# Kernel optimization log

Measured on AMD Instinct MI355X. Metric: run time of the kernel, lower is better.

The kernel has to match this reference:

```python
import jax, jax.numpy as jnp
import numpy as np

B, N, C = 4096, 49, 128
NUM_HEADS = 4
SCALE = C ** (-0.5)  # NOTE: source uses dim**-0.5, not head_dim**-0.5


def setup_inputs() -> dict:
    key = jax.random.key(0)
    k1, k2, k3 = jax.random.split(key, 3)
    x = jax.random.normal(k1, (B, N, C), dtype=jnp.float32)
    Wqkv = jax.random.normal(k2, (C, 3 * C), dtype=jnp.float32) * 0.02
    bqkv = jnp.zeros((3 * C,), dtype=jnp.float32)
    Wproj = jax.random.normal(k3, (C, C), dtype=jnp.float32) * 0.02
    bproj = jnp.zeros((C,), dtype=jnp.float32)
    return {"x": x, "Wqkv": Wqkv, "bqkv": bqkv, "Wproj": Wproj, "bproj": bproj}


def reference(x, Wqkv, bqkv, Wproj, bproj):
    b, n, c = x.shape
    h = NUM_HEADS
    d = c // h
    qkv = x @ Wqkv + bqkv                      # [B, N, 3C]
    qkv = qkv.reshape(b, n, 3, h, d).transpose(2, 0, 3, 1, 4)  # [3, B, H, N, d]
    q, k, v = qkv[0], qkv[1], qkv[2]
    attn = jnp.einsum("bhnd,bhmd->bhnm", q, k) * SCALE
    attn = jax.nn.softmax(attn, axis=-1)
    out = jnp.einsum("bhnm,bhmd->bhnd", attn, v)  # [B, H, N, d]
    out = out.transpose(0, 2, 1, 3).reshape(b, n, c)
    return out @ Wproj + bproj
```

## Files before the change

kernel.cpp:

```cpp
#include <hip/hip_runtime.h>


#define N_TOK 49
#define R1B 16384
#define SCF (0.08838834764831845f * 1.4426950408889634f)

typedef __attribute__((ext_vector_type(8))) __bf16 bf16x8;
typedef __attribute__((ext_vector_type(4))) __bf16 bf16x4;
typedef __attribute__((ext_vector_type(4))) float  f32x4;

__global__ void pack_weights(const float* __restrict__ Wqkv,
                             const float* __restrict__ Wproj,
                             __bf16* __restrict__ ws) {
    int idx  = blockIdx.x * 256 + threadIdx.x;
    int j    = idx & 7;
    int lane = (idx >> 3) & 63;
    int l16  = lane & 15, g = lane >> 4;
    if (idx < 49152) {
        int frag = idx >> 9;
        int mt = frag >> 2, ks = frag & 3;
        int m = mt * 16 + l16;
        int k = ks * 32 + g * 8 + j;
        float v = Wqkv[k * 384 + m];
        if (m < 128) v *= SCF;
        ws[idx] = (__bf16)v;
    } else {
        int i2 = idx - 49152;
        int frag = i2 >> 9;
        int nt = frag >> 2, ks = frag & 3;
        int n = nt * 16 + l16;
        int k = ks * 32 + g * 8 + j;
        ws[idx] = (__bf16)Wproj[k * 128 + n];
    }
}

__device__ __forceinline__ int x_off(int tok, int ch) {
    return tok * 256 + ((((ch >> 3) ^ (tok & 15))) << 4) + ((ch & 7) << 1);
}
__device__ __forceinline__ int vt_off(int h, int ch, int tok) {
    return h * 4096 + ch * 128 + ((((tok >> 3) ^ (ch & 7))) << 4) + ((tok & 7) << 1);
}
__device__ __forceinline__ int o_off(int tok, int ch) {
    return (ch >> 5) * 4096 + tok * 64 + (((((ch & 31) >> 3) ^ (tok & 3))) << 4) + ((ch & 7) << 1);
}
__device__ __forceinline__ int k_off(int h, int tok, int ch) {
    return R1B + h * 4096 + tok * 64 + ((((ch >> 3) ^ (tok & 3))) << 4) + ((ch & 7) << 1);
}

__device__ __forceinline__ int pk2(float a, float b) {
    union { __bf16 h[2]; int u; } U;
    U.h[0] = (__bf16)a; U.h[1] = (__bf16)b;
    return U.u;
}

__device__ __forceinline__ bf16x8 reorg8(int m0w0, int m0w1, int m1w0, int m1w1,
                                         int lane) {
    int aA = ((lane & 15) | ((lane & 16) << 1)) << 2;
    int aB = aA + 64;
    int A0 = __builtin_amdgcn_ds_bpermute(aA, m0w0);
    int A1 = __builtin_amdgcn_ds_bpermute(aA, m0w1);
    int B0 = __builtin_amdgcn_ds_bpermute(aB, m0w0);
    int B1 = __builtin_amdgcn_ds_bpermute(aB, m0w1);
    int C0 = __builtin_amdgcn_ds_bpermute(aA, m1w0);
    int C1 = __builtin_amdgcn_ds_bpermute(aA, m1w1);
    int D0 = __builtin_amdgcn_ds_bpermute(aB, m1w0);
    int D1 = __builtin_amdgcn_ds_bpermute(aB, m1w1);
    bool hi = lane >= 32;
    union { int u[4]; bf16x8 v; } U;
    U.u[0] = hi ? C0 : A0;
    U.u[1] = hi ? C1 : A1;
    U.u[2] = hi ? D0 : B0;
    U.u[3] = hi ? D1 : B1;
    return U.v;
}

__global__ __launch_bounds__(256, 4)
void fused_win_attn(const float* __restrict__ x,
                    const float* __restrict__ bqkv,
                    const float* __restrict__ bproj,
                    const __bf16* __restrict__ wpack,
                    float* __restrict__ out) {
    __shared__ __align__(16) char smem[32768];

    const int tid  = threadIdx.x;
    const int w    = tid >> 6;
    const int lane = tid & 63;
    const int l16  = lane & 15;
    const int g    = lane >> 4;
    const int b    = blockIdx.x;
    const float* xb = x + (size_t)b * (N_TOK * 128);

    #pragma unroll
    for (int it = 0; it < 4; ++it) {
        int unit = tid + it * 256;
        int tok = unit >> 4, ch = (unit & 15) * 8;
        f32x4 lo = {0.f, 0.f, 0.f, 0.f}, hi = {0.f, 0.f, 0.f, 0.f};
        if (tok < N_TOK) {
            const float* p = xb + tok * 128 + ch;
            lo = *(const f32x4*)p;
            hi = *(const f32x4*)(p + 4);
        }
        bf16x8 f;
        f[0]=(__bf16)lo[0]; f[1]=(__bf16)lo[1]; f[2]=(__bf16)lo[2]; f[3]=(__bf16)lo[3];
        f[4]=(__bf16)hi[0]; f[5]=(__bf16)hi[1]; f[6]=(__bf16)hi[2]; f[7]=(__bf16)hi[3];
        *(bf16x8*)(smem + x_off(tok, ch)) = f;
    }
    __syncthreads();

    f32x4 bq0 = *(const f32x4*)(bqkv + 32 * w + 0 + 4 * g);   bq0 *= SCF;
    f32x4 bq1 = *(const f32x4*)(bqkv + 32 * w + 16 + 4 * g);  bq1 *= SCF;
    f32x4 bk0 = *(const f32x4*)(bqkv + 128 + 32 * w + 0 + 4 * g);
    f32x4 bk1 = *(const f32x4*)(bqkv + 128 + 32 * w + 16 + 4 * g);
    f32x4 accA[4][4];
    #pragma unroll
    for (int nt = 0; nt < 4; ++nt) {
        accA[0][nt] = bq0; accA[1][nt] = bq1;
        accA[2][nt] = bk0; accA[3][nt] = bk1;
    }
    #pragma unroll
    for (int ks = 0; ks < 4; ++ks) {
        bf16x8 xfr[4];
        #pragma unroll
        for (int nt = 0; nt < 4; ++nt)
            xfr[nt] = *(const bf16x8*)(smem + x_off(16 * nt + l16, 32 * ks + 8 * g));
        #pragma unroll
        for (int m = 0; m < 4; ++m) {
            int mtg = (m < 2) ? (2 * w + m) : (8 + 2 * w + m - 2);
            bf16x8 af = *(const bf16x8*)(wpack + ((mtg * 4 + ks) * 64 + lane) * 8);
            #pragma unroll
            for (int nt = 0; nt < 4; ++nt)
                accA[m][nt] = __builtin_amdgcn_mfma_f32_16x16x32_bf16(af, xfr[nt], accA[m][nt], 0, 0, 0);
        }
    }
    #pragma unroll
    for (int m = 2; m < 4; ++m) {
        const int lch = 16 * (m - 2) + 4 * g;
        #pragma unroll
        for (int nt = 0; nt < 4; ++nt) {
            bf16x4 pk = {(__bf16)accA[m][nt][0], (__bf16)accA[m][nt][1],
                         (__bf16)accA[m][nt][2], (__bf16)accA[m][nt][3]};
            *(bf16x4*)(smem + k_off(w, 16 * nt + l16, lch)) = pk;
        }
    }
    bf16x8 qf[4];
    #pragma unroll
    for (int t = 0; t < 4; ++t) {
        int m0w0 = pk2(accA[0][t][0], accA[0][t][1]);
        int m0w1 = pk2(accA[0][t][2], accA[0][t][3]);
        int m1w0 = pk2(accA[1][t][0], accA[1][t][1]);
        int m1w1 = pk2(accA[1][t][2], accA[1][t][3]);
        qf[t] = reorg8(m0w0, m0w1, m1w0, m1w1, lane);
    }

    f32x4 bv0 = *(const f32x4*)(bqkv + 256 + 32 * w + 0 + 4 * g);
    f32x4 bv1 = *(const f32x4*)(bqkv + 256 + 32 * w + 16 + 4 * g);
    f32x4 accB[2][4];
    #pragma unroll
    for (int nt = 0; nt < 4; ++nt) { accB[0][nt] = bv0; accB[1][nt] = bv1; }
    #pragma unroll
    for (int ks = 0; ks < 4; ++ks) {
        bf16x8 xfr[4];
        #pragma unroll
        for (int nt = 0; nt < 4; ++nt)
            xfr[nt] = *(const bf16x8*)(smem + x_off(16 * nt + l16, 32 * ks + 8 * g));
        #pragma unroll
        for (int m = 0; m < 2; ++m) {
            bf16x8 af = *(const bf16x8*)(wpack + (((16 + 2 * w + m) * 4 + ks) * 64 + lane) * 8);
            #pragma unroll
            for (int nt = 0; nt < 4; ++nt)
                accB[m][nt] = __builtin_amdgcn_mfma_f32_16x16x32_bf16(af, xfr[nt], accB[m][nt], 0, 0, 0);
        }
    }
    __syncthreads();

    #pragma unroll
    for (int m = 0; m < 2; ++m) {
        const int vch = 16 * m + 4 * g;
        #pragma unroll
        for (int nt = 0; nt < 4; ++nt) {
            const int T = 16 * nt + l16;
            *(__bf16*)(smem + vt_off(w, vch + 0, T)) = (__bf16)accB[m][nt][0];
            *(__bf16*)(smem + vt_off(w, vch + 1, T)) = (__bf16)accB[m][nt][1];
            *(__bf16*)(smem + vt_off(w, vch + 2, T)) = (__bf16)accB[m][nt][2];
            *(__bf16*)(smem + vt_off(w, vch + 3, T)) = (__bf16)accB[m][nt][3];
        }
    }

    f32x4 s[4][4];
    #pragma unroll
    for (int mt = 0; mt < 4; ++mt) {
        bf16x8 kf = *(const bf16x8*)(smem + k_off(w, 16 * mt + l16, 8 * g));
        #pragma unroll
        for (int nt = 0; nt < 4; ++nt)
            s[mt][nt] = __builtin_amdgcn_mfma_f32_16x16x32_bf16(
                kf, qf[nt], (f32x4){0.f, 0.f, 0.f, 0.f}, 0, 0, 0);
    }

    float r[4];
    #pragma unroll
    for (int nt = 0; nt < 4; ++nt) {
        float sum = 0.f;
        #pragma unroll
        for (int mt = 0; mt < 4; ++mt)
            #pragma unroll
            for (int i = 0; i < 4; ++i) {
                int key = 16 * mt + 4 * g + i;
                float p = (key < N_TOK) ? __builtin_amdgcn_exp2f(s[mt][nt][i]) : 0.f;
                s[mt][nt][i] = p;
                sum += p;
            }
        sum += __shfl_xor(sum, 16);
        sum += __shfl_xor(sum, 32);
        r[nt] = __builtin_amdgcn_rcpf(sum);
    }

    bf16x8 pf[4][2];
    #pragma unroll
    for (int nt = 0; nt < 4; ++nt)
        #pragma unroll
        for (int ks = 0; ks < 2; ++ks) {
            int m0w0 = pk2(s[2 * ks][nt][0], s[2 * ks][nt][1]);
            int m0w1 = pk2(s[2 * ks][nt][2], s[2 * ks][nt][3]);
            int m1w0 = pk2(s[2 * ks + 1][nt][0], s[2 * ks + 1][nt][1]);
            int m1w1 = pk2(s[2 * ks + 1][nt][2], s[2 * ks + 1][nt][3]);
            pf[nt][ks] = reorg8(m0w0, m0w1, m1w0, m1w1, lane);
        }

    f32x4 o[2][4];
    #pragma unroll
    for (int m = 0; m < 2; ++m)
        #pragma unroll
        for (int nt = 0; nt < 4; ++nt) o[m][nt] = (f32x4){0.f, 0.f, 0.f, 0.f};
    #pragma unroll
    for (int ks = 0; ks < 2; ++ks)
        #pragma unroll
        for (int m = 0; m < 2; ++m) {
            bf16x8 vf = *(const bf16x8*)(smem + vt_off(w, 16 * m + l16, 32 * ks + 8 * g));
            #pragma unroll
            for (int nt = 0; nt < 4; ++nt)
                o[m][nt] = __builtin_amdgcn_mfma_f32_16x16x32_bf16(
                    vf, pf[nt][ks], o[m][nt], 0, 0, 0);
        }

    #pragma unroll
    for (int m = 0; m < 2; ++m)
        #pragma unroll
        for (int nt = 0; nt < 4; ++nt) {
            bf16x4 pk = {(__bf16)(o[m][nt][0] * r[nt]), (__bf16)(o[m][nt][1] * r[nt]),
                         (__bf16)(o[m][nt][2] * r[nt]), (__bf16)(o[m][nt][3] * r[nt])};
            *(bf16x4*)(smem + o_off(16 * nt + l16, 32 * w + 16 * m + 4 * g)) = pk;
        }

    const __bf16* bp = wpack + 49152;
    bf16x8 bpf[2][4];
    #pragma unroll
    for (int ntp = 0; ntp < 2; ++ntp)
        #pragma unroll
        for (int ks = 0; ks < 4; ++ks)
            bpf[ntp][ks] = *(const bf16x8*)(bp + (((2 * w + ntp) * 4 + ks) * 64 + lane) * 8);
    __syncthreads();

    const float bj0 = bproj[16 * (2 * w + 0) + l16];
    const float bj1 = bproj[16 * (2 * w + 1) + l16];
    f32x4 po[4][2];
    #pragma unroll
    for (int mt = 0; mt < 4; ++mt) {
        po[mt][0] = (f32x4){bj0, bj0, bj0, bj0};
        po[mt][1] = (f32x4){bj1, bj1, bj1, bj1};
    }
    #pragma unroll
    for (int ks = 0; ks < 4; ++ks) {
        #pragma unroll
        for (int mt = 0; mt < 4; ++mt) {
            bf16x8 a = *(const bf16x8*)(smem + o_off(16 * mt + l16, 32 * ks + 8 * g));
            po[mt][0] = __builtin_amdgcn_mfma_f32_16x16x32_bf16(a, bpf[0][ks], po[mt][0], 0, 0, 0);
            po[mt][1] = __builtin_amdgcn_mfma_f32_16x16x32_bf16(a, bpf[1][ks], po[mt][1], 0, 0, 0);
        }
    }
    #pragma unroll
    for (int ntp = 0; ntp < 2; ++ntp) {
        const int och = 16 * (2 * w + ntp) + l16;
        #pragma unroll
        for (int mt = 0; mt < 4; ++mt)
            #pragma unroll
            for (int i = 0; i < 4; ++i) {
                int tok = 16 * mt + 4 * g + i;
                if (tok < N_TOK)
                    out[((size_t)b * N_TOK + tok) * 128 + och] = po[mt][ntp][i];
            }
    }
}

extern "C" void kernel_launch(void* const* d_in, const int* in_sizes, int n_in,
                              void* d_out, int out_size, void* d_ws, size_t ws_size,
                              hipStream_t stream) {
    const float* x     = (const float*)d_in[0];
    const float* Wqkv  = (const float*)d_in[1];
    const float* bqkv  = (const float*)d_in[2];
    const float* Wproj = (const float*)d_in[3];
    const float* bproj = (const float*)d_in[4];
    __bf16* ws  = (__bf16*)d_ws;
    float* outp = (float*)d_out;

    pack_weights<<<256, 256, 0, stream>>>(Wqkv, Wproj, ws);
    fused_win_attn<<<4096, 256, 0, stream>>>(x, bqkv, bproj, ws, outp);
}
```

Before: 82.47 us.

## Split fused Q/K projection into separate passes and raise occupancy to 5 blocks

The combined Q+K projection, which held 16 f32x4 accumulators live at once, is split into a Q pass and a K pass. Each pass keeps only 8 accumulators, and K is written to shared memory before the V pass begins. Lowering peak register pressure is meant to fit launch_bounds(256,5), allowing more resident blocks per CU. The cost is that the X fragments are reloaded from LDS for an extra pass, and the tighter register budget could cause spills.

```diff
diff --git a/kernel.cpp b/kernel.cpp
--- a/kernel.cpp
+++ b/kernel.cpp
@@ -74,7 +74,7 @@
     return U.v;
 }
 
-__global__ __launch_bounds__(256, 4)
+__global__ __launch_bounds__(256, 5)
 void fused_win_attn(const float* __restrict__ x,
                     const float* __restrict__ bqkv,
                     const float* __restrict__ bproj,
@@ -107,15 +107,12 @@
     }
     __syncthreads();
 
-    f32x4 bq0 = *(const f32x4*)(bqkv + 32 * w + 0 + 4 * g);   bq0 *= SCF;
-    f32x4 bq1 = *(const f32x4*)(bqkv + 32 * w + 16 + 4 * g);  bq1 *= SCF;
-    f32x4 bk0 = *(const f32x4*)(bqkv + 128 + 32 * w + 0 + 4 * g);
-    f32x4 bk1 = *(const f32x4*)(bqkv + 128 + 32 * w + 16 + 4 * g);
-    f32x4 accA[4][4];
-    #pragma unroll
-    for (int nt = 0; nt < 4; ++nt) {
-        accA[0][nt] = bq0; accA[1][nt] = bq1;
-        accA[2][nt] = bk0; accA[3][nt] = bk1;
+    f32x4 accQ[2][4];
+    {
+        f32x4 bq0 = *(const f32x4*)(bqkv + 32 * w + 0 + 4 * g);   bq0 *= SCF;
+        f32x4 bq1 = *(const f32x4*)(bqkv + 32 * w + 16 + 4 * g);  bq1 *= SCF;
+        #pragma unroll
+        for (int nt = 0; nt < 4; ++nt) { accQ[0][nt] = bq0; accQ[1][nt] = bq1; }
     }
     #pragma unroll
     for (int ks = 0; ks < 4; ++ks) {
@@ -124,39 +121,62 @@
         for (int nt = 0; nt < 4; ++nt)
             xfr[nt] = *(const bf16x8*)(smem + x_off(16 * nt + l16, 32 * ks + 8 * g));
         #pragma unroll
-        for (int m = 0; m < 4; ++m) {
-            int mtg = (m < 2) ? (2 * w + m) : (8 + 2 * w + m - 2);
-            bf16x8 af = *(const bf16x8*)(wpack + ((mtg * 4 + ks) * 64 + lane) * 8);
+        for (int m = 0; m < 2; ++m) {
+            bf16x8 af = *(const bf16x8*)(wpack + (((2 * w + m) * 4 + ks) * 64 + lane) * 8);
             #pragma unroll
             for (int nt = 0; nt < 4; ++nt)
-                accA[m][nt] = __builtin_amdgcn_mfma_f32_16x16x32_bf16(af, xfr[nt], accA[m][nt], 0, 0, 0);
-        }
-    }
-    #pragma unroll
-    for (int m = 2; m < 4; ++m) {
-        const int lch = 16 * (m - 2) + 4 * g;
-        #pragma unroll
-        for (int nt = 0; nt < 4; ++nt) {
-            bf16x4 pk = {(__bf16)accA[m][nt][0], (__bf16)accA[m][nt][1],
-                         (__bf16)accA[m][nt][2], (__bf16)accA[m][nt][3]};
-            *(bf16x4*)(smem + k_off(w, 16 * nt + l16, lch)) = pk;
+                accQ[m][nt] = __builtin_amdgcn_mfma_f32_16x16x32_bf16(af, xfr[nt], accQ[m][nt], 0, 0, 0);
         }
     }
     bf16x8 qf[4];
     #pragma unroll
     for (int t = 0; t < 4; ++t) {
-        int m0w0 = pk2(accA[0][t][0], accA[0][t][1]);
-        int m0w1 = pk2(accA[0][t][2], accA[0][t][3]);
-        int m1w0 = pk2(accA[1][t][0], accA[1][t][1]);
-        int m1w1 = pk2(accA[1][t][2], accA[1][t][3]);
+        int m0w0 = pk2(accQ[0][t][0], accQ[0][t][1]);
+        int m0w1 = pk2(accQ[0][t][2], accQ[0][t][3]);
+        int m1w0 = pk2(accQ[1][t][0], accQ[1][t][1]);
+        int m1w1 = pk2(accQ[1][t][2], accQ[1][t][3]);
         qf[t] = reorg8(m0w0, m0w1, m1w0, m1w1, lane);
     }
 
-    f32x4 bv0 = *(const f32x4*)(bqkv + 256 + 32 * w + 0 + 4 * g);
-    f32x4 bv1 = *(const f32x4*)(bqkv + 256 + 32 * w + 16 + 4 * g);
+    {
+        f32x4 accK[2][4];
+        f32x4 bk0 = *(const f32x4*)(bqkv + 128 + 32 * w + 0 + 4 * g);
+        f32x4 bk1 = *(const f32x4*)(bqkv + 128 + 32 * w + 16 + 4 * g);
+        #pragma unroll
+        for (int nt = 0; nt < 4; ++nt) { accK[0][nt] = bk0; accK[1][nt] = bk1; }
+        #pragma unroll
+        for (int ks = 0; ks < 4; ++ks) {
+            bf16x8 xfr[4];
+            #pragma unroll
+            for (int nt = 0; nt < 4; ++nt)
+                xfr[nt] = *(const bf16x8*)(smem + x_off(16 * nt + l16, 32 * ks + 8 * g));
+            #pragma unroll
+            for (int m = 0; m < 2; ++m) {
+                bf16x8 af = *(const bf16x8*)(wpack + (((8 + 2 * w + m) * 4 + ks) * 64 + lane) * 8);
+                #pragma unroll
+                for (int nt = 0; nt < 4; ++nt)
+                    accK[m][nt] = __builtin_amdgcn_mfma_f32_16x16x32_bf16(af, xfr[nt], accK[m][nt], 0, 0, 0);
+            }
+        }
+        #pragma unroll
+        for (int m = 0; m < 2; ++m) {
+            const int lch = 16 * m + 4 * g;
+            #pragma unroll
+            for (int nt = 0; nt < 4; ++nt) {
+                bf16x4 pk = {(__bf16)accK[m][nt][0], (__bf16)accK[m][nt][1],
+                             (__bf16)accK[m][nt][2], (__bf16)accK[m][nt][3]};
+                *(bf16x4*)(smem + k_off(w, 16 * nt + l16, lch)) = pk;
+            }
+        }
+    }
+
     f32x4 accB[2][4];
-    #pragma unroll
-    for (int nt = 0; nt < 4; ++nt) { accB[0][nt] = bv0; accB[1][nt] = bv1; }
+    {
+        f32x4 bv0 = *(const f32x4*)(bqkv + 256 + 32 * w + 0 + 4 * g);
+        f32x4 bv1 = *(const f32x4*)(bqkv + 256 + 32 * w + 16 + 4 * g);
+        #pragma unroll
+        for (int nt = 0; nt < 4; ++nt) { accB[0][nt] = bv0; accB[1][nt] = bv1; }
+    }
     #pragma unroll
     for (int ks = 0; ks < 4; ++ks) {
         bf16x8 xfr[4];
```

Result: slower. 152.5 us (+84.9%).
